# Optimization experiments

Hardware: AMD Instinct MI355X
Metric: run time of the kernel (lower is better)

The kernel has to match this reference:

```python
import jax, jax.numpy as jnp
import numpy as np
from jax import lax

SQRT_HALF = 0.7071067811865476
LAYERS = 20
STACKS = 2
LAYERS_PER_STACK = LAYERS // STACKS
K = 3
OUT_CH = 256
RES_CH = 64
GATE_CH = 128
SKIP_CH = 256
CIN_CH = 80


def setup_inputs() -> dict:
    key = jax.random.key(0)
    ks = jax.random.split(key, 20)
    s = 0.05
    inp = {
        'x': jax.random.normal(ks[0], (4, OUT_CH, 16384), jnp.float32),
        'c': jax.random.normal(ks[1], (4, CIN_CH, 16384), jnp.float32),
        # first conv: kernel size 2 (Conv1d2x1), out_channels -> residual_channels
        'W_first': jax.random.normal(ks[2], (RES_CH, OUT_CH, 2), jnp.float32) * s,
        'b_first': jnp.zeros((RES_CH,), jnp.float32),
        # per-layer dilated conv (residual -> gate), stacked over layers
        'W_dil': jax.random.normal(ks[3], (LAYERS, GATE_CH, RES_CH, K), jnp.float32) * s,
        'b_dil': jnp.zeros((LAYERS, GATE_CH), jnp.float32),
        # per-layer local-conditioning 1x1 (cin -> gate)
        'W_c': jax.random.normal(ks[4], (LAYERS, GATE_CH, CIN_CH), jnp.float32) * s,
        'b_c': jnp.zeros((LAYERS, GATE_CH), jnp.float32),
        # per-layer 1x1 skip (gate/2 -> skip) and out (gate/2 -> residual)
        'W_skip': jax.random.normal(ks[5], (LAYERS, SKIP_CH, GATE_CH // 2), jnp.float32) * s,
        'b_skip': jnp.zeros((LAYERS, SKIP_CH), jnp.float32),
        'W_out': jax.random.normal(ks[6], (LAYERS, RES_CH, GATE_CH // 2), jnp.float32) * s,
        'b_out': jnp.zeros((LAYERS, RES_CH), jnp.float32),
        # final 1x1 convs
        'W_last1': jax.random.normal(ks[7], (SKIP_CH, SKIP_CH), jnp.float32) * s,
        'b_last1': jnp.zeros((SKIP_CH,), jnp.float32),
        'W_last2': jax.random.normal(ks[8], (OUT_CH, SKIP_CH), jnp.float32) * s,
        'b_last2': jnp.zeros((OUT_CH,), jnp.float32),
    }
    return inp


def reference(x, c, W_first, b_first, W_dil, b_dil, W_c, b_c,
              W_skip, b_skip, W_out, b_out, W_last1, b_last1, W_last2, b_last2):
    dn = ('NCH', 'OIH', 'NCH')
    # first conv: F.pad(x, (1,0)) then kernel-2 conv == causal left pad 1
    h = lax.conv_general_dilated(x, W_first, (1,), [(1, 0)], dimension_numbers=dn)
    h = jnp.tanh(h + b_first[None, :, None])  # hparams.use_tanh_embed
    skips = None
    for l in range(LAYERS):
        d = 2 ** (l % LAYERS_PER_STACK)
        # causal dilated conv: pad left (K-1)*d
        y = lax.conv_general_dilated(h, W_dil[l], (1,), [((K - 1) * d, 0)],
                                     rhs_dilation=(d,), dimension_numbers=dn)
        y = y + b_dil[l][None, :, None]
        cond = jnp.einsum('bct,gc->bgt', c, W_c[l]) + b_c[l][None, :, None]
        a, b = jnp.split(y + cond, 2, axis=1)  # gated activation units
        z = jnp.tanh(a) * jax.nn.sigmoid(b)
        s = jnp.einsum('bgt,sg->bst', z, W_skip[l]) + b_skip[l][None, :, None]
        h = (jnp.einsum('bgt,rg->brt', z, W_out[l]) + b_out[l][None, :, None] + h) * SQRT_HALF
        if skips is None:
            skips = s
        else:
            skips = (skips + s) * SQRT_HALF  # faithful to original accumulation
    out = jax.nn.relu(skips)
    out = jnp.einsum('bst,os->bot', out, W_last1) + b_last1[None, :, None]
    out = jax.nn.relu(out)
    out = jnp.einsum('bst,os->bot', out, W_last2) + b_last2[None, :, None]
    return out
```

## Files before the change

kernel.cpp:

```cpp
#include <hip/hip_runtime.h>
#include <math.h>


#define T_LEN   16384
#define NB      4
#define BT      (NB * T_LEN)
#define NLAYERS 20
#define SQH     0.70710678118654752440f

typedef _Float16 half8 __attribute__((ext_vector_type(8)));
typedef _Float16 half4 __attribute__((ext_vector_type(4)));
typedef float f32x4 __attribute__((ext_vector_type(4)));

__device__ inline f32x4 mfma16(half8 a, half8 b, f32x4 c) {
  return __builtin_amdgcn_mfma_f32_16x16x32_f16(a, b, c, 0, 0, 0);
}

__device__ __forceinline__ int xswz(int pb, int nwg) {
  return (pb & 7) * (nwg >> 3) + (pb >> 3);
}

__global__ __launch_bounds__(256) void prep_pack(
    const float* __restrict__ Wf, const float* __restrict__ Wdil,
    const float* __restrict__ Wc, const float* __restrict__ Wskip,
    const float* __restrict__ Wout, const float* __restrict__ Wl1,
    const float* __restrict__ Wl2, const float* __restrict__ bdil,
    const float* __restrict__ bc, const float* __restrict__ bskip,
    _Float16* __restrict__ wdp, _Float16* __restrict__ wcp,
    _Float16* __restrict__ wop, _Float16* __restrict__ wskp,
    _Float16* __restrict__ wfp, _Float16* __restrict__ wl1p,
    _Float16* __restrict__ wl2p, float* __restrict__ bde,
    float* __restrict__ bsk)
{
  const float Q = 0.70710678118654752440f;
  const int WDP_E = 20 * 3 * 128 * 64;
  const int WCP_E = 20 * 128 * 96;
  const int WOP_E = 20 * 64 * 64;
  const int WSK_E = 256 * 1280;
  const int WFP_E = 64 * 512;
  const int WL_E  = 256 * 256;
  const int BDE_E = 20 * 128;
  const int BSK_E = 256;
  const int TOTAL = WDP_E + WCP_E + WOP_E + WSK_E + WFP_E + 2 * WL_E + BDE_E + BSK_E;
  for (int i = blockIdx.x * blockDim.x + threadIdx.x; i < TOTAL;
       i += gridDim.x * blockDim.x) {
    int j = i;
    if (j < WDP_E) {
      int l = j / (3 * 128 * 64); int r2 = j % (3 * 128 * 64);
      int tau = r2 / (128 * 64);  int r3 = r2 % (128 * 64);
      int n = r3 >> 6; int kc = r3 & 63;
      wdp[j] = (_Float16)Wdil[((l * 128 + n) * 64 + kc) * 3 + tau];
      continue;
    }
    j -= WDP_E;
    if (j < WCP_E) {
      int l = j / (128 * 96); int r2 = j % (128 * 96);
      int n = r2 / 96; int kc = r2 % 96;
      wcp[j] = (_Float16)(kc < 80 ? Wc[(l * 128 + n) * 80 + kc] : 0.f);
      continue;
    }
    j -= WCP_E;
    if (j < WOP_E) {
      int l = j >> 12; int r2 = j & 4095;
      int n = r2 >> 6; int kc = r2 & 63;
      wop[j] = (_Float16)Wout[(l * 64 + n) * 64 + kc];
      continue;
    }
    j -= WOP_E;
    if (j < WSK_E) {
      int n = j / 1280; int k = j % 1280;
      int l = k >> 6; int kc = k & 63;
      float f = (l == 0) ? 1.f : powf(Q, (float)(1 - l));
      wskp[j] = (_Float16)(Wskip[(l * 256 + n) * 64 + kc] * f);
      continue;
    }
    j -= WSK_E;
    if (j < WFP_E) {
      int n = j >> 9; int k = j & 511;
      int tau = k >> 8; int ci = k & 255;
      wfp[j] = (_Float16)Wf[(n * 256 + ci) * 2 + tau];
      continue;
    }
    j -= WFP_E;
    if (j < WL_E) { wl1p[j] = (_Float16)Wl1[j]; continue; }
    j -= WL_E;
    if (j < WL_E) { wl2p[j] = (_Float16)Wl2[j]; continue; }
    j -= WL_E;
    if (j < BDE_E) { bde[j] = bdil[j] + bc[j]; continue; }
    j -= BDE_E;
    {
      int n = j;
      float s = 0.f;
      for (int l = 0; l < NLAYERS; ++l) {
        float w = powf(Q, (float)(l == 0 ? 19 : 20 - l));
        s += bskip[l * 256 + n] * w;
      }
      bsk[n] = s;
    }
  }
}

__global__ __launch_bounds__(256) void tr_x_kernel(
    const float* __restrict__ src, _Float16* __restrict__ dst)
{
  __shared__ float tile[32 * 132];
  const int lb = xswz(blockIdx.x, 4096);
  const int row_tile = lb >> 3, cb = lb & 7;
  const int bb = row_tile >> 7;
  const int t0 = (row_tile & 127) * 128;
  const int ch0 = cb * 32;
  {
    int ch = threadIdx.x >> 3, tq = (threadIdx.x & 7) * 16;
    const float4* s4 = (const float4*)(src + ((size_t)(bb * 256 + ch0 + ch)) * T_LEN + t0 + tq);
#pragma unroll
    for (int j = 0; j < 4; ++j)
      *(float4*)&tile[ch * 132 + tq + 4 * j] = s4[j];
  }
  __syncthreads();
  {
    int t = threadIdx.x >> 1, c16 = (threadIdx.x & 1) * 16;
    half8 h0, h1;
#pragma unroll
    for (int j = 0; j < 8; ++j) {
      h0[j] = (_Float16)tile[(c16 + j) * 132 + t];
      h1[j] = (_Float16)tile[(c16 + 8 + j) * 132 + t];
    }
    _Float16* o = dst + ((size_t)(bb * T_LEN + t0 + t)) * 256 + ch0 + c16;
    *(half8*)o = h0;
    *(half8*)(o + 8) = h1;
  }
}

__global__ __launch_bounds__(256) void tr_kernel(
    const float* __restrict__ src, _Float16* __restrict__ dst, int C, int Cpad, int CB)
{
  __shared__ float tile[32 * 33];
  int lb = xswz(blockIdx.x, gridDim.x);
  int cb = lb % CB;
  int tb = (lb / CB) % (T_LEN / 32);
  int bb = lb / (CB * (T_LEN / 32));
  int t0 = tb * 32, ch0 = cb * 32;
  int tl = threadIdx.x & 31, cl = threadIdx.x >> 5;
#pragma unroll
  for (int i = 0; i < 4; ++i) {
    int ch = cl + 8 * i;
    float v = (ch0 + ch < C) ? src[((size_t)bb * C + ch0 + ch) * T_LEN + t0 + tl] : 0.f;
    tile[ch * 33 + tl] = v;
  }
  __syncthreads();
  int t = threadIdx.x >> 3;
  int c4 = (threadIdx.x & 7) * 4;
  half4 hv = {(_Float16)tile[(c4 + 0) * 33 + t], (_Float16)tile[(c4 + 1) * 33 + t],
              (_Float16)tile[(c4 + 2) * 33 + t], (_Float16)tile[(c4 + 3) * 33 + t]};
  *(half4*)&dst[((size_t)bb * T_LEN + t0 + t) * Cpad + ch0 + c4] = hv;
}

__global__ __launch_bounds__(256, 4) void first_conv(
    const _Float16* __restrict__ xt, const _Float16* __restrict__ wfp,
    const float* __restrict__ bf, _Float16* __restrict__ h0)
{
  __shared__ _Float16 As[128 * 72];
  __shared__ _Float16 Bs[64 * 72];
  const int tid = threadIdx.x;
  const int lane = tid & 63, w = tid >> 6;
  const int wx = w & 1, wy = w >> 1;
  const int l15 = lane & 15, quad = lane >> 4;
  const int p0 = xswz(blockIdx.x, 512) * 128;
  const int b = p0 >> 14, t0 = p0 & (T_LEN - 1);
  const int r = tid >> 1, halfo = (tid & 1) * 32;

  f32x4 acc[4][2];
#pragma unroll
  for (int mi = 0; mi < 4; ++mi)
#pragma unroll
    for (int ni = 0; ni < 2; ++ni) { f32x4 z = {0.f, 0.f, 0.f, 0.f}; acc[mi][ni] = z; }

  for (int s = 0; s < 8; ++s) {
    int tau = s >> 2, ci0 = (s & 3) * 64;
    int ts = t0 + r - 1 + tau;
    if (ts >= 0) {
      const uint4* src = (const uint4*)(xt + ((size_t)(b * T_LEN + ts) * 256 + ci0 + halfo));
#pragma unroll
      for (int j = 0; j < 4; ++j) *(uint4*)&As[r * 72 + halfo + 8 * j] = src[j];
    } else {
      uint4 z = {0, 0, 0, 0};
#pragma unroll
      for (int j = 0; j < 4; ++j) *(uint4*)&As[r * 72 + halfo + 8 * j] = z;
    }
    if (tid < 128) {
      const uint4* s4 = (const uint4*)(wfp + ((size_t)r * 512 + tau * 256 + ci0 + halfo));
#pragma unroll
      for (int j = 0; j < 4; ++j) *(uint4*)&Bs[r * 72 + halfo + 8 * j] = s4[j];
    }
    __syncthreads();
#pragma unroll
    for (int kc = 0; kc < 2; ++kc) {
      const int k0 = kc * 32 + quad * 8;
      half8 af[4], bfr[2];
#pragma unroll
      for (int mi = 0; mi < 4; ++mi)
        af[mi] = *(const half8*)&As[(64 * wy + 16 * mi + l15) * 72 + k0];
#pragma unroll
      for (int ni = 0; ni < 2; ++ni)
        bfr[ni] = *(const half8*)&Bs[(32 * wx + 16 * ni + l15) * 72 + k0];
#pragma unroll
      for (int mi = 0; mi < 4; ++mi)
#pragma unroll
        for (int ni = 0; ni < 2; ++ni)
          acc[mi][ni] = mfma16(af[mi], bfr[ni], acc[mi][ni]);
    }
    __syncthreads();
  }
#pragma unroll
  for (int mi = 0; mi < 4; ++mi)
#pragma unroll
    for (int ni = 0; ni < 2; ++ni) {
      int col = 32 * wx + 16 * ni + l15;
      int rowb = 64 * wy + 16 * mi + quad * 4;
      float bo = bf[col];
      size_t base = ((size_t)p0 + rowb) * 64 + col;
#pragma unroll
      for (int reg = 0; reg < 4; ++reg) {
        float v = acc[mi][ni][reg] + bo;
        float e = __expf(2.f * v);
        h0[base + (size_t)64 * reg] = (_Float16)(1.f - 2.f * __builtin_amdgcn_rcpf(e + 1.f));
      }
    }
}

__global__ __launch_bounds__(512, 4) void layer_kernel(
    const _Float16* __restrict__ hprev, _Float16* __restrict__ hnext,
    const _Float16* __restrict__ ctp,
    const _Float16* __restrict__ wdp_l, const _Float16* __restrict__ wcp_l,
    const _Float16* __restrict__ wop_l,
    const float* __restrict__ bde_l, const float* __restrict__ bout_l,
    _Float16* __restrict__ zslot, int d, int last)
{
  __shared__ _Float16 As[128 * 72];
  __shared__ _Float16 Bs[128 * 72];
  __shared__ float bde_s[128];

  const int tid = threadIdx.x;
  const int lane = tid & 63, w = tid >> 6;
  const int wx = w & 1, wy = w >> 1;
  const int l15 = lane & 15, quad = lane >> 4;
  const int p0 = xswz(blockIdx.x, 512) * 128;
  const int b = p0 >> 14, t0 = p0 & (T_LEN - 1);
  const int r2 = tid >> 2, qo = (tid & 3) * 16;
  const int o8 = (tid & 3) * 8;

  if (tid < 128) bde_s[tid] = bde_l[tid];

  f32x4 acc[2][4];
#pragma unroll
  for (int mi = 0; mi < 2; ++mi)
#pragma unroll
    for (int ni = 0; ni < 4; ++ni) { f32x4 z = {0.f, 0.f, 0.f, 0.f}; acc[mi][ni] = z; }

  for (int s = 0; s < 5; ++s) {
    if (s < 3) {
      int ts = t0 + r2 - (2 - s) * d;
      if (ts >= 0) {
        const uint4* src = (const uint4*)(hprev + ((size_t)(b * T_LEN + ts) * 64 + qo));
        *(uint4*)&As[r2 * 72 + qo] = src[0];
        *(uint4*)&As[r2 * 72 + qo + 8] = src[1];
      } else {
        uint4 z4 = {0, 0, 0, 0};
        *(uint4*)&As[r2 * 72 + qo] = z4;
        *(uint4*)&As[r2 * 72 + qo + 8] = z4;
      }
      const uint4* sb = (const uint4*)(wdp_l + ((size_t)s * 8192 + r2 * 64 + qo));
      *(uint4*)&Bs[r2 * 72 + qo] = sb[0];
      *(uint4*)&Bs[r2 * 72 + qo + 8] = sb[1];
    } else if (s == 3) {
      const uint4* sa = (const uint4*)(ctp + ((size_t)(p0 + r2) * 96 + qo));
      *(uint4*)&As[r2 * 72 + qo] = sa[0];
      *(uint4*)&As[r2 * 72 + qo + 8] = sa[1];
      const uint4* sb = (const uint4*)(wcp_l + ((size_t)r2 * 96 + qo));
      *(uint4*)&Bs[r2 * 72 + qo] = sb[0];
      *(uint4*)&Bs[r2 * 72 + qo + 8] = sb[1];
    } else {
      *(uint4*)&As[r2 * 72 + o8] = *(const uint4*)(ctp + ((size_t)(p0 + r2) * 96 + 64 + o8));
      *(uint4*)&Bs[r2 * 72 + o8] = *(const uint4*)(wcp_l + ((size_t)r2 * 96 + 64 + o8));
    }
    __syncthreads();
    const int nkc = (s == 4) ? 1 : 2;
    for (int kc = 0; kc < nkc; ++kc) {
      const int k0 = kc * 32 + quad * 8;
      half8 af[2], bfr[4];
#pragma unroll
      for (int mi = 0; mi < 2; ++mi)
        af[mi] = *(const half8*)&As[(32 * wy + 16 * mi + l15) * 72 + k0];
#pragma unroll
      for (int ni = 0; ni < 4; ++ni) {
        int ncol = 32 * wx + 16 * (ni & 1) + 64 * (ni >> 1);
        bfr[ni] = *(const half8*)&Bs[(ncol + l15) * 72 + k0];
      }
#pragma unroll
      for (int mi = 0; mi < 2; ++mi)
#pragma unroll
        for (int ni = 0; ni < 4; ++ni)
          acc[mi][ni] = mfma16(af[mi], bfr[ni], acc[mi][ni]);
    }
    __syncthreads();
  }

#pragma unroll
  for (int mi = 0; mi < 2; ++mi)
#pragma unroll
    for (int ni2 = 0; ni2 < 2; ++ni2) {
      int colb = 32 * wx + 16 * ni2 + l15;
      float ba = bde_s[colb], bb = bde_s[colb + 64];
#pragma unroll
      for (int reg = 0; reg < 4; ++reg) {
        float av = acc[mi][ni2][reg] + ba;
        float gv = acc[mi][ni2 + 2][reg] + bb;
        float ea = __expf(2.f * av);
        float th = 1.f - 2.f * __builtin_amdgcn_rcpf(ea + 1.f);
        float sg = __builtin_amdgcn_rcpf(1.f + __expf(-gv));
        As[(32 * wy + 16 * mi + quad * 4 + reg) * 72 + colb] = (_Float16)(th * sg);
      }
    }

  if (!last && tid < 256) {
    int row = tid >> 2;
    const uint4* sb = (const uint4*)(wop_l + ((size_t)row * 64 + qo));
    *(uint4*)&Bs[row * 72 + qo] = sb[0];
    *(uint4*)&Bs[row * 72 + qo + 8] = sb[1];
  }
  __syncthreads();

  {
    uint4 v0 = *(const uint4*)&As[r2 * 72 + qo];
    uint4 v1 = *(const uint4*)&As[r2 * 72 + qo + 8];
    uint4* dst = (uint4*)(zslot + ((size_t)(p0 + r2) * 64 + qo));
    dst[0] = v0; dst[1] = v1;
  }

  if (last) return;

  f32x4 a4[2][2];
#pragma unroll
  for (int mi = 0; mi < 2; ++mi)
#pragma unroll
    for (int ni = 0; ni < 2; ++ni) { f32x4 z = {0.f, 0.f, 0.f, 0.f}; a4[mi][ni] = z; }
#pragma unroll
  for (int kc = 0; kc < 2; ++kc) {
    const int k0 = kc * 32 + quad * 8;
    half8 af[2], bfr[2];
#pragma unroll
    for (int mi = 0; mi < 2; ++mi)
      af[mi] = *(const half8*)&As[(32 * wy + 16 * mi + l15) * 72 + k0];
#pragma unroll
    for (int ni = 0; ni < 2; ++ni)
      bfr[ni] = *(const half8*)&Bs[(32 * wx + 16 * ni + l15) * 72 + k0];
#pragma unroll
    for (int mi = 0; mi < 2; ++mi)
#pragma unroll
      for (int ni = 0; ni < 2; ++ni)
        a4[mi][ni] = mfma16(af[mi], bfr[ni], a4[mi][ni]);
  }
#pragma unroll
  for (int mi = 0; mi < 2; ++mi)
#pragma unroll
    for (int ni = 0; ni < 2; ++ni) {
      int col = 32 * wx + 16 * ni + l15;
      int rowb = 32 * wy + 16 * mi + quad * 4;
      float bo = bout_l[col];
      size_t base = ((size_t)p0 + rowb) * 64 + col;
#pragma unroll
      for (int reg = 0; reg < 4; ++reg) {
        float hv = (float)hprev[base + (size_t)64 * reg];
        hnext[base + (size_t)64 * reg] = (_Float16)((a4[mi][ni][reg] + bo + hv) * SQH);
      }
    }
}

__global__ __launch_bounds__(512, 4) void flush_kernel(
    const _Float16* __restrict__ zbuf, const _Float16* __restrict__ wskp,
    _Float16* __restrict__ Abuf, const float* __restrict__ bsk,
    _Float16* __restrict__ skr, int l0, int g, int mode)
{
  __shared__ _Float16 As[128 * 72];
  __shared__ _Float16 Bs0[128 * 72];
  __shared__ _Float16 Bs1[128 * 72];
  const int tid = threadIdx.x;
  const int half = tid >> 8;
  _Float16* Bsh = half ? Bs1 : Bs0;
  const int tloc = tid & 255;
  const int lane = tloc & 63, w4 = tloc >> 6;
  const int wx = w4 & 1, wy = w4 >> 1;
  const int l15 = lane & 15, quad = lane >> 4;
  const int p0 = xswz(blockIdx.x, 512) * 128;
  const int n0 = half * 128;
  const int r = tloc >> 1, halfo = (tloc & 1) * 32;

  f32x4 acc[4][4];
#pragma unroll
  for (int mi = 0; mi < 4; ++mi)
#pragma unroll
    for (int ni = 0; ni < 4; ++ni) { f32x4 z = {0.f, 0.f, 0.f, 0.f}; acc[mi][ni] = z; }

#pragma unroll 1
  for (int j = 0; j < g; ++j) {
    const int lj = l0 + j;
    const _Float16* zsl = zbuf + (size_t)(lj & 7) * ((size_t)BT * 64);
    if (half == 0) {
      const uint4* sa = (const uint4*)(zsl + ((size_t)(p0 + r) * 64 + halfo));
#pragma unroll
      for (int jj = 0; jj < 4; ++jj) *(uint4*)&As[r * 72 + halfo + 8 * jj] = sa[jj];
    }
    const uint4* sb = (const uint4*)(wskp + ((size_t)(n0 + r) * 1280 + lj * 64 + halfo));
#pragma unroll
    for (int jj = 0; jj < 4; ++jj) *(uint4*)&Bsh[r * 72 + halfo + 8 * jj] = sb[jj];
    __syncthreads();
#pragma unroll
    for (int kc = 0; kc < 2; ++kc) {
      const int k0 = kc * 32 + quad * 8;
      half8 af[4], bfr[4];
#pragma unroll
      for (int mi = 0; mi < 4; ++mi)
        af[mi] = *(const half8*)&As[(64 * wy + 16 * mi + l15) * 72 + k0];
#pragma unroll
      for (int ni = 0; ni < 4; ++ni)
        bfr[ni] = *(const half8*)&Bsh[(64 * wx + 16 * ni + l15) * 72 + k0];
#pragma unroll
      for (int mi = 0; mi < 4; ++mi)
#pragma unroll
        for (int ni = 0; ni < 4; ++ni)
          acc[mi][ni] = mfma16(af[mi], bfr[ni], acc[mi][ni]);
    }
    __syncthreads();
  }
  const float Q19 = 0.0013810679320049757f;
#pragma unroll
  for (int mi = 0; mi < 4; ++mi)
#pragma unroll
    for (int ni = 0; ni < 4; ++ni) {
      int col = n0 + 64 * wx + 16 * ni + l15;
      int rowb = 64 * wy + 16 * mi + quad * 4;
      size_t base = ((size_t)p0 + rowb) * 256 + col;
      if (mode == 2) {
        float bb = bsk[col];
#pragma unroll
        for (int reg = 0; reg < 4; ++reg) {
          float v = (acc[mi][ni][reg] + (float)Abuf[base + (size_t)256 * reg]) * Q19 + bb;
          skr[base + (size_t)256 * reg] = (_Float16)(v > 0.f ? v : 0.f);
        }
      } else if (mode == 1) {
#pragma unroll
        for (int reg = 0; reg < 4; ++reg) {
          size_t a = base + (size_t)256 * reg;
          Abuf[a] = (_Float16)((float)Abuf[a] + acc[mi][ni][reg]);
        }
      } else {
#pragma unroll
        for (int reg = 0; reg < 4; ++reg)
          Abuf[base + (size_t)256 * reg] = (_Float16)acc[mi][ni][reg];
      }
    }
}

__global__ __launch_bounds__(256, 4) void gemm256(
    const _Float16* __restrict__ Asrc, const _Float16* __restrict__ Bp,
    const float* __restrict__ bias, void* __restrict__ dst, int mode)
{
  __shared__ _Float16 smem[2 * 128 * 72];
  _Float16* As = smem;
  _Float16* Bs = smem + 128 * 72;
  const int tid = threadIdx.x;
  const int lane = tid & 63, w = tid >> 6;
  const int wx = w & 1, wy = w >> 1;
  const int l15 = lane & 15, quad = lane >> 4;
  const int p0 = xswz(blockIdx.x, 512) * 128;
  const int n0 = blockIdx.y * 128;
  const int r = tid >> 1, halfo = (tid & 1) * 32;

  f32x4 acc[4][4];
#pragma unroll
  for (int mi = 0; mi < 4; ++mi)
#pragma unroll
    for (int ni = 0; ni < 4; ++ni) { f32x4 z = {0.f, 0.f, 0.f, 0.f}; acc[mi][ni] = z; }

  for (int c4 = 0; c4 < 4; ++c4) {
    int k0g = c4 * 64;
    const uint4* sa = (const uint4*)(Asrc + ((size_t)(p0 + r) * 256 + k0g + halfo));
#pragma unroll
    for (int jj = 0; jj < 4; ++jj) *(uint4*)&As[r * 72 + halfo + 8 * jj] = sa[jj];
    const uint4* sb = (const uint4*)(Bp + ((size_t)(n0 + r) * 256 + k0g + halfo));
#pragma unroll
    for (int jj = 0; jj < 4; ++jj) *(uint4*)&Bs[r * 72 + halfo + 8 * jj] = sb[jj];
    __syncthreads();
#pragma unroll
    for (int kc = 0; kc < 2; ++kc) {
      const int k0 = kc * 32 + quad * 8;
      half8 af[4], bfr[4];
#pragma unroll
      for (int mi = 0; mi < 4; ++mi)
        af[mi] = *(const half8*)&As[(64 * wy + 16 * mi + l15) * 72 + k0];
#pragma unroll
      for (int ni = 0; ni < 4; ++ni)
        bfr[ni] = *(const half8*)&Bs[(64 * wx + 16 * ni + l15) * 72 + k0];
#pragma unroll
      for (int mi = 0; mi < 4; ++mi)
#pragma unroll
        for (int ni = 0; ni < 4; ++ni)
          acc[mi][ni] = mfma16(af[mi], bfr[ni], acc[mi][ni]);
    }
    __syncthreads();
  }
  if (mode == 0) {
#pragma unroll
    for (int mi = 0; mi < 4; ++mi)
#pragma unroll
      for (int ni = 0; ni < 4; ++ni) {
        int col = n0 + 64 * wx + 16 * ni + l15;
        int rowb = 64 * wy + 16 * mi + quad * 4;
        float bv = bias[col];
        _Float16* o = (_Float16*)dst;
#pragma unroll
        for (int reg = 0; reg < 4; ++reg) {
          float v = acc[mi][ni][reg] + bv;
          o[((size_t)(p0 + rowb + reg)) * 256 + col] = (_Float16)(v > 0.f ? v : 0.f);
        }
      }
  } else {
    float* Ts = (float*)smem;
    const int b = p0 >> 14, t0g = p0 & (T_LEN - 1);
    for (int pass = 0; pass < 2; ++pass) {
      if (wx == pass) {
#pragma unroll
        for (int mi = 0; mi < 4; ++mi)
#pragma unroll
          for (int ni = 0; ni < 4; ++ni) {
            int col_l = 16 * ni + l15;
            float bv = bias[n0 + 64 * pass + col_l];
            int tl = 64 * wy + 16 * mi + quad * 4;
#pragma unroll
            for (int reg = 0; reg < 4; ++reg)
              Ts[col_l * 132 + tl + reg] = acc[mi][ni][reg] + bv;
          }
      }
      __syncthreads();
      {
        int col_l = tid >> 2;
        int tq = (tid & 3) * 32;
        float* o = (float*)dst + ((size_t)b * 256 + n0 + 64 * pass + col_l) * T_LEN + t0g + tq;
#pragma unroll
        for (int j = 0; j < 8; ++j)
          *(float4*)(o + 4 * j) = *(const float4*)&Ts[col_l * 132 + tq + 4 * j];
      }
      __syncthreads();
    }
  }
}

extern "C" void kernel_launch(void* const* d_in, const int* in_sizes, int n_in,
                              void* d_out, int out_size, void* d_ws, size_t ws_size,
                              hipStream_t stream)
{
  const float* x     = (const float*)d_in[0];
  const float* c     = (const float*)d_in[1];
  const float* Wf    = (const float*)d_in[2];
  const float* bf    = (const float*)d_in[3];
  const float* Wdil  = (const float*)d_in[4];
  const float* bdil  = (const float*)d_in[5];
  const float* Wc    = (const float*)d_in[6];
  const float* bc    = (const float*)d_in[7];
  const float* Wskip = (const float*)d_in[8];
  const float* bskip = (const float*)d_in[9];
  const float* Wout  = (const float*)d_in[10];
  const float* bout  = (const float*)d_in[11];
  const float* Wl1   = (const float*)d_in[12];
  const float* bl1   = (const float*)d_in[13];
  const float* Wl2   = (const float*)d_in[14];
  const float* bl2   = (const float*)d_in[15];

  char* base = (char*)d_ws;
  _Float16* zbuf = (_Float16*)base;
  _Float16* xt   = zbuf;
  _Float16* skr  = zbuf + (size_t)4 * BT * 64;
  _Float16* y1   = zbuf;
  _Float16* ctp  = (_Float16*)(base + 67108864);
  _Float16* hA   = (_Float16*)(base + 79691776);
  _Float16* hB   = (_Float16*)(base + 88080384);
  _Float16* wdp  = (_Float16*)(base + 96468992);
  _Float16* wcp  = wdp  + (size_t)20 * 3 * 128 * 64;
  _Float16* wop  = wcp  + (size_t)20 * 128 * 96;
  _Float16* wskp = wop  + (size_t)20 * 64 * 64;
  _Float16* wfp  = wskp + (size_t)256 * 1280;
  _Float16* wl1p = wfp  + (size_t)64 * 512;
  _Float16* wl2p = wl1p + (size_t)256 * 256;
  float*    bde  = (float*)(wl2p + (size_t)256 * 256);
  float*    bsk  = bde + 20 * 128;
  _Float16* Abuf = (_Float16*)d_out;

  prep_pack<<<2048, 256, 0, stream>>>(Wf, Wdil, Wc, Wskip, Wout, Wl1, Wl2,
                                      bdil, bc, bskip,
                                      wdp, wcp, wop, wskp, wfp, wl1p, wl2p,
                                      bde, bsk);
  tr_x_kernel<<<4096, 256, 0, stream>>>(x, xt);
  tr_kernel<<<NB * (T_LEN / 32) * 3, 256, 0, stream>>>(c, ctp, 80, 96, 3);
  first_conv<<<512, 256, 0, stream>>>(xt, wfp, bf, hA);

  const _Float16* hin = hA;
  _Float16* hout = hB;
  for (int l = 0; l < NLAYERS; ++l) {
    int d = 1 << (l % 10);
    layer_kernel<<<512, 512, 0, stream>>>(
        hin, hout, ctp,
        wdp + (size_t)l * 3 * 128 * 64, wcp + (size_t)l * 128 * 96,
        wop + (size_t)l * 64 * 64, bde + l * 128, bout + l * 64,
        zbuf + (size_t)(l & 7) * BT * 64, d, (l == NLAYERS - 1) ? 1 : 0);
    _Float16* tmp = (_Float16*)hin; hin = hout; hout = tmp;
    if (l == 7)  flush_kernel<<<512, 512, 0, stream>>>(zbuf, wskp, Abuf, bsk, skr, 0, 8, 0);
    if (l == 15) flush_kernel<<<512, 512, 0, stream>>>(zbuf, wskp, Abuf, bsk, skr, 8, 8, 1);
    if (l == 19) flush_kernel<<<512, 512, 0, stream>>>(zbuf, wskp, Abuf, bsk, skr, 16, 4, 2);
  }
  gemm256<<<dim3(512, 2), 256, 0, stream>>>(skr, wl1p, bl1, (void*)y1, 0);
  gemm256<<<dim3(512, 2), 256, 0, stream>>>(y1, wl2p, bl2, d_out, 1);
}
```

Before: 617.1 us.

## Fuse skip flush GEMM into layer kernel and stage epilogue stores through LDS

Removes the three separate flush_kernel launches and runs the skip-projection accumulation inside the layer kernel on layers 7, 15 and 19, reusing the same block's row tile. The flush handles both 128-column halves sequentially with one shared B buffer. Epilogues in first_conv, layer_kernel, the flush and gemm256 mode 0 now stage results in shared memory and write coalesced 16-byte rows instead of scattered 2-byte stores. This cuts launch count and global write inefficiency, but the flush-carrying layers run longer per block, with more syncs and larger register arrays.

```diff
diff --git a/kernel.cpp b/kernel.cpp
--- a/kernel.cpp
+++ b/kernel.cpp
@@ -218,14 +218,21 @@
       int col = 32 * wx + 16 * ni + l15;
       int rowb = 64 * wy + 16 * mi + quad * 4;
       float bo = bf[col];
-      size_t base = ((size_t)p0 + rowb) * 64 + col;
 #pragma unroll
       for (int reg = 0; reg < 4; ++reg) {
         float v = acc[mi][ni][reg] + bo;
         float e = __expf(2.f * v);
-        h0[base + (size_t)64 * reg] = (_Float16)(1.f - 2.f * __builtin_amdgcn_rcpf(e + 1.f));
-      }
-    }
+        As[(rowb + reg) * 72 + col] = (_Float16)(1.f - 2.f * __builtin_amdgcn_rcpf(e + 1.f));
+      }
+    }
+  __syncthreads();
+  {
+    int row = tid >> 1, co = (tid & 1) * 32;
+    _Float16* o = h0 + ((size_t)(p0 + row)) * 64 + co;
+    const uint4* s = (const uint4*)&As[row * 72 + co];
+#pragma unroll
+    for (int j = 0; j < 4; ++j) *(uint4*)(o + 8 * j) = s[j];
+  }
 }
 
 __global__ __launch_bounds__(512, 4) void layer_kernel(
@@ -234,11 +241,15 @@
     const _Float16* __restrict__ wdp_l, const _Float16* __restrict__ wcp_l,
     const _Float16* __restrict__ wop_l,
     const float* __restrict__ bde_l, const float* __restrict__ bout_l,
-    _Float16* __restrict__ zslot, int d, int last)
+    _Float16* __restrict__ zslot, int d, int last,
+    const _Float16* __restrict__ zbuf, const _Float16* __restrict__ wskp,
+    _Float16* __restrict__ Abuf, const float* __restrict__ bsk,
+    _Float16* __restrict__ skr, int fl0, int fg, int fmode)
 {
-  __shared__ _Float16 As[128 * 72];
-  __shared__ _Float16 Bs[128 * 72];
+  __shared__ _Float16 smem[2 * 128 * 72];
   __shared__ float bde_s[128];
+  _Float16* As = smem;
+  _Float16* Bs = smem + 128 * 72;
 
   const int tid = threadIdx.x;
   const int lane = tid & 63, w = tid >> 6;
@@ -337,128 +348,157 @@
     dst[0] = v0; dst[1] = v1;
   }
 
-  if (last) return;
-
-  f32x4 a4[2][2];
-#pragma unroll
-  for (int mi = 0; mi < 2; ++mi)
-#pragma unroll
-    for (int ni = 0; ni < 2; ++ni) { f32x4 z = {0.f, 0.f, 0.f, 0.f}; a4[mi][ni] = z; }
-#pragma unroll
-  for (int kc = 0; kc < 2; ++kc) {
-    const int k0 = kc * 32 + quad * 8;
-    half8 af[2], bfr[2];
+  if (!last) {
+    f32x4 a4[2][2];
 #pragma unroll
     for (int mi = 0; mi < 2; ++mi)
-      af[mi] = *(const half8*)&As[(32 * wy + 16 * mi + l15) * 72 + k0];
-#pragma unroll
-    for (int ni = 0; ni < 2; ++ni)
-      bfr[ni] = *(const half8*)&Bs[(32 * wx + 16 * ni + l15) * 72 + k0];
-#pragma unroll
-    for (int mi = 0; mi < 2; ++mi)
-#pragma unroll
-      for (int ni = 0; ni < 2; ++ni)
-        a4[mi][ni] = mfma16(af[mi], bfr[ni], a4[mi][ni]);
-  }
-#pragma unroll
-  for (int mi = 0; mi < 2; ++mi)
-#pragma unroll
-    for (int ni = 0; ni < 2; ++ni) {
-      int col = 32 * wx + 16 * ni + l15;
-      int rowb = 32 * wy + 16 * mi + quad * 4;
-      float bo = bout_l[col];
-      size_t base = ((size_t)p0 + rowb) * 64 + col;
-#pragma unroll
-      for (int reg = 0; reg < 4; ++reg) {
-        float hv = (float)hprev[base + (size_t)64 * reg];
-        hnext[base + (size_t)64 * reg] = (_Float16)((a4[mi][ni][reg] + bo + hv) * SQH);
-      }
-    }
-}
-
-__global__ __launch_bounds__(512, 4) void flush_kernel(
-    const _Float16* __restrict__ zbuf, const _Float16* __restrict__ wskp,
-    _Float16* __restrict__ Abuf, const float* __restrict__ bsk,
-    _Float16* __restrict__ skr, int l0, int g, int mode)
-{
-  __shared__ _Float16 As[128 * 72];
-  __shared__ _Float16 Bs0[128 * 72];
-  __shared__ _Float16 Bs1[128 * 72];
-  const int tid = threadIdx.x;
-  const int half = tid >> 8;
-  _Float16* Bsh = half ? Bs1 : Bs0;
-  const int tloc = tid & 255;
-  const int lane = tloc & 63, w4 = tloc >> 6;
-  const int wx = w4 & 1, wy = w4 >> 1;
-  const int l15 = lane & 15, quad = lane >> 4;
-  const int p0 = xswz(blockIdx.x, 512) * 128;
-  const int n0 = half * 128;
-  const int r = tloc >> 1, halfo = (tloc & 1) * 32;
-
-  f32x4 acc[4][4];
-#pragma unroll
-  for (int mi = 0; mi < 4; ++mi)
-#pragma unroll
-    for (int ni = 0; ni < 4; ++ni) { f32x4 z = {0.f, 0.f, 0.f, 0.f}; acc[mi][ni] = z; }
-
-#pragma unroll 1
-  for (int j = 0; j < g; ++j) {
-    const int lj = l0 + j;
-    const _Float16* zsl = zbuf + (size_t)(lj & 7) * ((size_t)BT * 64);
-    if (half == 0) {
-      const uint4* sa = (const uint4*)(zsl + ((size_t)(p0 + r) * 64 + halfo));
-#pragma unroll
-      for (int jj = 0; jj < 4; ++jj) *(uint4*)&As[r * 72 + halfo + 8 * jj] = sa[jj];
-    }
-    const uint4* sb = (const uint4*)(wskp + ((size_t)(n0 + r) * 1280 + lj * 64 + halfo));
-#pragma unroll
-    for (int jj = 0; jj < 4; ++jj) *(uint4*)&Bsh[r * 72 + halfo + 8 * jj] = sb[jj];
-    __syncthreads();
+#pragma unroll
+      for (int ni = 0; ni < 2; ++ni) { f32x4 z = {0.f, 0.f, 0.f, 0.f}; a4[mi][ni] = z; }
 #pragma unroll
     for (int kc = 0; kc < 2; ++kc) {
       const int k0 = kc * 32 + quad * 8;
-      half8 af[4], bfr[4];
-#pragma unroll
-      for (int mi = 0; mi < 4; ++mi)
-        af[mi] = *(const half8*)&As[(64 * wy + 16 * mi + l15) * 72 + k0];
-#pragma unroll
-      for (int ni = 0; ni < 4; ++ni)
-        bfr[ni] = *(const half8*)&Bsh[(64 * wx + 16 * ni + l15) * 72 + k0];
-#pragma unroll
-      for (int mi = 0; mi < 4; ++mi)
+      half8 af[2], bfr[2];
+#pragma unroll
+      for (int mi = 0; mi < 2; ++mi)
+        af[mi] = *(const half8*)&As[(32 * wy + 16 * mi + l15) * 72 + k0];
+#pragma unroll
+      for (int ni = 0; ni < 2; ++ni)
+        bfr[ni] = *(const half8*)&Bs[(32 * wx + 16 * ni + l15) * 72 + k0];
+#pragma unroll
+      for (int mi = 0; mi < 2; ++mi)
+#pragma unroll
+        for (int ni = 0; ni < 2; ++ni)
+          a4[mi][ni] = mfma16(af[mi], bfr[ni], a4[mi][ni]);
+    }
+    __syncthreads();
+#pragma unroll
+    for (int mi = 0; mi < 2; ++mi)
+#pragma unroll
+      for (int ni = 0; ni < 2; ++ni) {
+        int col = 32 * wx + 16 * ni + l15;
+        int rowb = 32 * wy + 16 * mi + quad * 4;
+        float bo = bout_l[col];
+        size_t base = ((size_t)p0 + rowb) * 64 + col;
+#pragma unroll
+        for (int reg = 0; reg < 4; ++reg) {
+          float hv = (float)hprev[base + (size_t)64 * reg];
+          As[(rowb + reg) * 72 + col] = (_Float16)((a4[mi][ni][reg] + bo + hv) * SQH);
+        }
+      }
+    __syncthreads();
+    {
+      uint4 v0 = *(const uint4*)&As[r2 * 72 + qo];
+      uint4 v1 = *(const uint4*)&As[r2 * 72 + qo + 8];
+      uint4* dst = (uint4*)(hnext + ((size_t)(p0 + r2) * 64 + qo));
+      dst[0] = v0; dst[1] = v1;
+    }
+  }
+
+  if (fmode >= 0) {
+    __syncthreads();
+    __threadfence_block();
+    f32x4 fac[2][2][4];
+#pragma unroll
+    for (int p = 0; p < 2; ++p)
+#pragma unroll
+      for (int mi = 0; mi < 2; ++mi)
+#pragma unroll
+        for (int ni = 0; ni < 4; ++ni) { f32x4 z = {0.f, 0.f, 0.f, 0.f}; fac[p][mi][ni] = z; }
+
+#pragma unroll 1
+    for (int j = 0; j < fg; ++j) {
+      const int lj = fl0 + j;
+      const _Float16* zsl = zbuf + (size_t)(lj & 7) * ((size_t)BT * 64);
+      {
+        const uint4* sa = (const uint4*)(zsl + ((size_t)(p0 + r2) * 64 + qo));
+        *(uint4*)&As[r2 * 72 + qo] = sa[0];
+        *(uint4*)&As[r2 * 72 + qo + 8] = sa[1];
+        const uint4* sb = (const uint4*)(wskp + ((size_t)r2 * 1280 + lj * 64 + qo));
+        *(uint4*)&Bs[r2 * 72 + qo] = sb[0];
+        *(uint4*)&Bs[r2 * 72 + qo + 8] = sb[1];
+      }
+      __syncthreads();
+#pragma unroll
+      for (int kc = 0; kc < 2; ++kc) {
+        const int k0 = kc * 32 + quad * 8;
+        half8 af[2], bfr[4];
+#pragma unroll
+        for (int mi = 0; mi < 2; ++mi)
+          af[mi] = *(const half8*)&As[(32 * wy + 16 * mi + l15) * 72 + k0];
 #pragma unroll
         for (int ni = 0; ni < 4; ++ni)
-          acc[mi][ni] = mfma16(af[mi], bfr[ni], acc[mi][ni]);
-    }
-    __syncthreads();
-  }
-  const float Q19 = 0.0013810679320049757f;
-#pragma unroll
-  for (int mi = 0; mi < 4; ++mi)
-#pragma unroll
-    for (int ni = 0; ni < 4; ++ni) {
-      int col = n0 + 64 * wx + 16 * ni + l15;
-      int rowb = 64 * wy + 16 * mi + quad * 4;
-      size_t base = ((size_t)p0 + rowb) * 256 + col;
-      if (mode == 2) {
-        float bb = bsk[col];
-#pragma unroll
-        for (int reg = 0; reg < 4; ++reg) {
-          float v = (acc[mi][ni][reg] + (float)Abuf[base + (size_t)256 * reg]) * Q19 + bb;
-          skr[base + (size_t)256 * reg] = (_Float16)(v > 0.f ? v : 0.f);
-        }
-      } else if (mode == 1) {
-#pragma unroll
-        for (int reg = 0; reg < 4; ++reg) {
-          size_t a = base + (size_t)256 * reg;
-          Abuf[a] = (_Float16)((float)Abuf[a] + acc[mi][ni][reg]);
-        }
-      } else {
-#pragma unroll
-        for (int reg = 0; reg < 4; ++reg)
-          Abuf[base + (size_t)256 * reg] = (_Float16)acc[mi][ni][reg];
-      }
-    }
+          bfr[ni] = *(const half8*)&Bs[(64 * wx + 16 * ni + l15) * 72 + k0];
+#pragma unroll
+        for (int mi = 0; mi < 2; ++mi)
+#pragma unroll
+          for (int ni = 0; ni < 4; ++ni)
+            fac[0][mi][ni] = mfma16(af[mi], bfr[ni], fac[0][mi][ni]);
+      }
+      __syncthreads();
+      {
+        const uint4* sb = (const uint4*)(wskp + ((size_t)(128 + r2) * 1280 + lj * 64 + qo));
+        *(uint4*)&Bs[r2 * 72 + qo] = sb[0];
+        *(uint4*)&Bs[r2 * 72 + qo + 8] = sb[1];
+      }
+      __syncthreads();
+#pragma unroll
+      for (int kc = 0; kc < 2; ++kc) {
+        const int k0 = kc * 32 + quad * 8;
+        half8 af[2], bfr[4];
+#pragma unroll
+        for (int mi = 0; mi < 2; ++mi)
+          af[mi] = *(const half8*)&As[(32 * wy + 16 * mi + l15) * 72 + k0];
+#pragma unroll
+        for (int ni = 0; ni < 4; ++ni)
+          bfr[ni] = *(const half8*)&Bs[(64 * wx + 16 * ni + l15) * 72 + k0];
+#pragma unroll
+        for (int mi = 0; mi < 2; ++mi)
+#pragma unroll
+          for (int ni = 0; ni < 4; ++ni)
+            fac[1][mi][ni] = mfma16(af[mi], bfr[ni], fac[1][mi][ni]);
+      }
+      __syncthreads();
+    }
+
+    const float Q19 = 0.0013810679320049757f;
+    _Float16* Ts = smem;
+    _Float16* dbase = (fmode == 2) ? skr : Abuf;
+#pragma unroll 1
+    for (int h = 0; h < 2; ++h) {
+      if ((wy >> 1) == h) {
+#pragma unroll
+        for (int p = 0; p < 2; ++p)
+#pragma unroll
+          for (int mi = 0; mi < 2; ++mi)
+#pragma unroll
+            for (int ni = 0; ni < 4; ++ni) {
+              int col = p * 128 + 64 * wx + 16 * ni + l15;
+              int rowb = 32 * wy + 16 * mi + quad * 4;
+#pragma unroll
+              for (int reg = 0; reg < 4; ++reg) {
+                int row = rowb + reg;
+                float v = fac[p][mi][ni][reg];
+                if (fmode == 1) {
+                  v += (float)Abuf[((size_t)(p0 + row)) * 256 + col];
+                } else if (fmode == 2) {
+                  v = (v + (float)Abuf[((size_t)(p0 + row)) * 256 + col]) * Q19 + bsk[col];
+                  v = v > 0.f ? v : 0.f;
+                }
+                Ts[(row - 64 * h) * 264 + col] = (_Float16)v;
+              }
+            }
+      }
+      __syncthreads();
+      {
+        int lr = tid >> 3, co = (tid & 7) * 32;
+        _Float16* o = dbase + ((size_t)(p0 + 64 * h + lr)) * 256 + co;
+        const uint4* s = (const uint4*)&Ts[lr * 264 + co];
+#pragma unroll
+        for (int jj = 0; jj < 4; ++jj) *(uint4*)(o + 8 * jj) = s[jj];
+      }
+      __syncthreads();
+    }
+  }
 }
 
 __global__ __launch_bounds__(256, 4) void gemm256(
@@ -510,20 +550,34 @@
     __syncthreads();
   }
   if (mode == 0) {
-#pragma unroll
-    for (int mi = 0; mi < 4; ++mi)
-#pragma unroll
-      for (int ni = 0; ni < 4; ++ni) {
-        int col = n0 + 64 * wx + 16 * ni + l15;
-        int rowb = 64 * wy + 16 * mi + quad * 4;
-        float bv = bias[col];
-        _Float16* o = (_Float16*)dst;
-#pragma unroll
-        for (int reg = 0; reg < 4; ++reg) {
-          float v = acc[mi][ni][reg] + bv;
-          o[((size_t)(p0 + rowb + reg)) * 256 + col] = (_Float16)(v > 0.f ? v : 0.f);
-        }
-      }
+    _Float16* Ts = smem;
+#pragma unroll 1
+    for (int h = 0; h < 2; ++h) {
+      if (wy == h) {
+#pragma unroll
+        for (int mi = 0; mi < 4; ++mi)
+#pragma unroll
+          for (int ni = 0; ni < 4; ++ni) {
+            int col = 64 * wx + 16 * ni + l15;
+            int lr = 16 * mi + quad * 4;
+            float bv = bias[n0 + col];
+#pragma unroll
+            for (int reg = 0; reg < 4; ++reg) {
+              float v = acc[mi][ni][reg] + bv;
+              Ts[(lr + reg) * 136 + col] = (_Float16)(v > 0.f ? v : 0.f);
+            }
+          }
+      }
+      __syncthreads();
+      {
+        int lr = tid >> 2, co = (tid & 3) * 32;
+        _Float16* o = (_Float16*)dst + ((size_t)(p0 + 64 * h + lr)) * 256 + n0 + co;
+        const uint4* s = (const uint4*)&Ts[lr * 136 + co];
+#pragma unroll
+        for (int jj = 0; jj < 4; ++jj) *(uint4*)(o + 8 * jj) = s[jj];
+      }
+      __syncthreads();
+    }
   } else {
     float* Ts = (float*)smem;
     const int b = p0 >> 14, t0g = p0 & (T_LEN - 1);
@@ -607,15 +661,16 @@
   _Float16* hout = hB;
   for (int l = 0; l < NLAYERS; ++l) {
     int d = 1 << (l % 10);
+    int fm  = (l == 7) ? 0 : (l == 15) ? 1 : (l == NLAYERS - 1) ? 2 : -1;
+    int fl0 = (l == 7) ? 0 : (l == 15) ? 8 : 16;
+    int fg  = (l == NLAYERS - 1) ? 4 : 8;
     layer_kernel<<<512, 512, 0, stream>>>(
         hin, hout, ctp,
         wdp + (size_t)l * 3 * 128 * 64, wcp + (size_t)l * 128 * 96,
         wop + (size_t)l * 64 * 64, bde + l * 128, bout + l * 64,
-        zbuf + (size_t)(l & 7) * BT * 64, d, (l == NLAYERS - 1) ? 1 : 0);
+        zbuf + (size_t)(l & 7) * BT * 64, d, (l == NLAYERS - 1) ? 1 : 0,
+        zbuf, wskp, Abuf, bsk, skr, fl0, fg, fm);
     _Float16* tmp = (_Float16*)hin; hin = hout; hout = tmp;
-    if (l == 7)  flush_kernel<<<512, 512, 0, stream>>>(zbuf, wskp, Abuf, bsk, skr, 0, 8, 0);
-    if (l == 15) flush_kernel<<<512, 512, 0, stream>>>(zbuf, wskp, Abuf, bsk, skr, 8, 8, 1);
-    if (l == 19) flush_kernel<<<512, 512, 0, stream>>>(zbuf, wskp, Abuf, bsk, skr, 16, 4, 2);
   }
   gemm256<<<dim3(512, 2), 256, 0, stream>>>(skr, wl1p, bl1, (void*)y1, 0);
   gemm256<<<dim3(512, 2), 256, 0, stream>>>(y1, wl2p, bl2, d_out, 1);
```

Measured after the change: 675.0 us. 9.4% more time.
